# Optimization experiments

Measured on AMD Instinct MI355X. Metric: run time of the kernel, lower is better.

## Reference

```python
import jax, jax.numpy as jnp
import numpy as np

K = 8  # avg_kernel (pool kernel == stride, and nearest-upsample factor)


def conv1x1(u, W, b):
    # 1x1 conv == per-pixel linear map over channels
    return jnp.einsum('bchw,oc->bohw', u, W) + b[None, :, None, None]


def setup_inputs() -> dict:
    key = jax.random.key(0)
    ks = jax.random.split(key, 9)
    C = 64
    x = jax.random.normal(ks[0], (8, C, 512, 512), dtype=jnp.float32)
    def w(k):
        return jax.random.normal(k, (C, C), dtype=jnp.float32) * 0.05
    def bias(k):
        return jax.random.normal(k, (C,), dtype=jnp.float32) * 0.05
    return {
        'x': x,
        'Wt': w(ks[1]), 'bt': bias(ks[2]),
        'Wp': w(ks[3]), 'bp': bias(ks[4]),
        'Wg': w(ks[5]), 'bg': bias(ks[6]),
        'Wc': w(ks[7]), 'bc': bias(ks[8]),
    }


def reference(x, Wt, bt, Wp, bp, Wg, bg, Wc, bc):
    B, C, H, W = x.shape
    # AvgPool2d(kernel=K, stride=K): exact reshape-mean since H,W divisible by K
    u = x.reshape(B, C, H // K, K, W // K, K).mean(axis=(3, 5))  # [B,C,h,w]
    b_, c_, h, w_ = u.shape
    N = h * w_
    theta = conv1x1(u, Wt, bt).reshape(B, C, N).transpose(0, 2, 1)  # [B,N,C]
    phi = conv1x1(u, Wp, bp).reshape(B, C, N)                       # [B,C,N] (downsample = flatten)
    g = conv1x1(u, Wg, bg).reshape(B, C, N).transpose(0, 2, 1)      # [B,N,C]
    attn = jax.nn.softmax(jnp.einsum('bnc,bcm->bnm', theta, phi), axis=-1)  # [B,N,N], unscaled
    y = jnp.einsum('bnm,bmc->bnc', attn, g)                         # [B,N,C]
    y = y.transpose(0, 2, 1).reshape(B, C, h, w_)
    y = conv1x1(y, Wc, bc)
    # F.interpolate(size=[H,W]) default nearest; integer factor K -> exact repeat
    y = jnp.repeat(jnp.repeat(y, K, axis=2), K, axis=3)
    return y
```

## Files before the change

kernel.cpp:

```cpp
#include <hip/hip_runtime.h>
#include <hip/hip_bf16.h>


typedef short short8 __attribute__((ext_vector_type(8)));
typedef float floatx4 __attribute__((ext_vector_type(4)));

__device__ inline unsigned short f2bf(float f) {
    union { float f; unsigned int u; } v; v.f = f;
    unsigned int u = v.u;
    u += 0x7fff + ((u >> 16) & 1);
    return (unsigned short)(u >> 16);
}

__device__ inline float rowsum16(float x) {
    x += __int_as_float(__builtin_amdgcn_update_dpp(0, __float_as_int(x), 0x121, 0xf, 0xf, false));
    x += __int_as_float(__builtin_amdgcn_update_dpp(0, __float_as_int(x), 0x122, 0xf, 0xf, false));
    x += __int_as_float(__builtin_amdgcn_update_dpp(0, __float_as_int(x), 0x124, 0xf, 0xf, false));
    x += __int_as_float(__builtin_amdgcn_update_dpp(0, __float_as_int(x), 0x128, 0xf, 0xf, false));
    return x;
}

__global__ __launch_bounds__(256) void k_pool(const float* __restrict__ x,
                                              float* __restrict__ u) {
    int id = blockIdx.x * 256 + threadIdx.x;
    int ow = id & 63;
    int oh = (id >> 6) & 63;
    int bc = id >> 12;
    const float* p = x + ((size_t)bc * 512 + oh * 8) * 512 + ow * 8;
    float s = 0.f;
#pragma unroll
    for (int r = 0; r < 8; ++r) {
        const float4* q = (const float4*)(p + r * 512);
        float4 a = q[0], b = q[1];
        s += a.x + a.y + a.z + a.w + b.x + b.y + b.z + b.w;
    }
    u[id] = s * (1.f / 64.f);
}

__global__ __launch_bounds__(256) void k_qkv(const float* __restrict__ u,
    const float* __restrict__ Wt, const float* __restrict__ bt,
    const float* __restrict__ Wp, const float* __restrict__ bp,
    const float* __restrict__ Wg, const float* __restrict__ bg,
    unsigned short* __restrict__ th, unsigned short* __restrict__ ph,
    unsigned short* __restrict__ gT) {
    __shared__ float U[64 * 66];
    __shared__ float WtT[64 * 64];
    __shared__ float WpT[64 * 64];
    int b = blockIdx.x >> 6;
    int n0 = (blockIdx.x & 63) * 64;
    int t = threadIdx.x;
#pragma unroll
    for (int i = 0; i < 4; ++i) {
        int f4 = t + 256 * i;
        int cin = f4 >> 4, pos = f4 & 15;
        float4 v = *(const float4*)(u + ((size_t)(b * 64 + cin)) * 4096 + n0 + pos * 4);
        U[cin * 66 + pos * 4 + 0] = v.x;
        U[cin * 66 + pos * 4 + 1] = v.y;
        U[cin * 66 + pos * 4 + 2] = v.z;
        U[cin * 66 + pos * 4 + 3] = v.w;
    }
#pragma unroll
    for (int i = 0; i < 16; ++i) {
        int idx = t + 256 * i;
        int co = idx & 63, ci = idx >> 6;
        WtT[ci * 64 + co] = Wt[co * 64 + ci];
        WpT[ci * 64 + co] = Wp[co * 64 + ci];
    }
    __syncthreads();
    int cO = t & 63, wv = t >> 6;
#pragma unroll 4
    for (int i = 0; i < 16; ++i) {
        int nl = wv + 4 * i;
        float at = bt[cO], ap = bp[cO];
#pragma unroll
        for (int cin = 0; cin < 64; ++cin) {
            float uv = U[cin * 66 + nl];
            at += WtT[cin * 64 + cO] * uv;
            ap += WpT[cin * 64 + cO] * uv;
        }
        size_t o = ((size_t)(b * 4096 + n0 + nl)) * 64 + cO;
        th[o] = f2bf(at);
        ph[o] = f2bf(ap);
    }
#pragma unroll 4
    for (int i = 0; i < 16; ++i) {
        int c = wv + 4 * i;
        float ag = bg[c];
#pragma unroll
        for (int cin = 0; cin < 64; ++cin)
            ag += Wg[c * 64 + cin] * U[cin * 66 + (t & 63)];
        gT[((size_t)(b * 64 + c)) * 4096 + n0 + (t & 63)] = f2bf(ag);
    }
}

__global__ __launch_bounds__(256) void k_attn(
    const unsigned short* __restrict__ th,
    const unsigned short* __restrict__ ph,
    const unsigned short* __restrict__ gT,
    float* __restrict__ y) {
    __shared__ unsigned short Th[64 * 72];
    __shared__ unsigned short Ph[2][64 * 72];
    __shared__ unsigned short Gt[2][64 * 72];
    __shared__ unsigned short Pl[4 * 16 * 72];
    int b = blockIdx.x >> 6;
    int n0 = (blockIdx.x & 63) * 64;
    int t = threadIdx.x;
    int wave = t >> 6, lane = t & 63, quad = lane >> 4, l16 = lane & 15;
    int row = t >> 2, cg = t & 3;

    {
        const unsigned short* src = th + ((size_t)(b * 4096 + n0 + row)) * 64;
        *(short8*)(Th + row * 72 + cg * 8)      = *(const short8*)(src + cg * 8);
        *(short8*)(Th + row * 72 + 32 + cg * 8) = *(const short8*)(src + 32 + cg * 8);
        const unsigned short* sp = ph + ((size_t)(b * 4096 + row)) * 64;
        *(short8*)(Ph[0] + row * 72 + cg * 8)      = *(const short8*)(sp + cg * 8);
        *(short8*)(Ph[0] + row * 72 + 32 + cg * 8) = *(const short8*)(sp + 32 + cg * 8);
        const unsigned short* sg = gT + ((size_t)(b * 64 + row)) * 4096;
        *(short8*)(Gt[0] + row * 72 + cg * 8)      = *(const short8*)(sg + cg * 8);
        *(short8*)(Gt[0] + row * 72 + 32 + cg * 8) = *(const short8*)(sg + 32 + cg * 8);
    }
    __syncthreads();
    short8 a0 = *(const short8*)(Th + (wave * 16 + l16) * 72 + quad * 8);
    short8 a1 = *(const short8*)(Th + (wave * 16 + l16) * 72 + 32 + quad * 8);

    floatx4 Yacc[4];
#pragma unroll
    for (int ct = 0; ct < 4; ++ct) Yacc[ct] = (floatx4){0.f, 0.f, 0.f, 0.f};
    float l[4] = {0.f, 0.f, 0.f, 0.f};

    int cur = 0;
    for (int mt = 0; mt < 64; ++mt) {
        int mn = ((mt + 1) & 63) * 64;
        short8 r0, r1, r2, r3;
        {
            const unsigned short* sp = ph + ((size_t)(b * 4096 + mn + row)) * 64;
            r0 = *(const short8*)(sp + cg * 8);
            r1 = *(const short8*)(sp + 32 + cg * 8);
            const unsigned short* sg = gT + ((size_t)(b * 64 + row)) * 4096 + mn;
            r2 = *(const short8*)(sg + cg * 8);
            r3 = *(const short8*)(sg + 32 + cg * 8);
        }
        const unsigned short* PhC = Ph[cur];
        const unsigned short* GtC = Gt[cur];

        float psum[4] = {0.f, 0.f, 0.f, 0.f};
#pragma unroll
        for (int ct = 0; ct < 4; ++ct) {
            short8 b0 = *(const short8*)(PhC + (ct * 16 + l16) * 72 + quad * 8);
            short8 b1 = *(const short8*)(PhC + (ct * 16 + l16) * 72 + 32 + quad * 8);
            floatx4 acc = (floatx4){0.f, 0.f, 0.f, 0.f};
            __builtin_amdgcn_s_setprio(1);
            acc = __builtin_amdgcn_mfma_f32_16x16x32_bf16(a0, b0, acc, 0, 0, 0);
            acc = __builtin_amdgcn_mfma_f32_16x16x32_bf16(a1, b1, acc, 0, 0, 0);
            __builtin_amdgcn_s_setprio(0);
#pragma unroll
            for (int r = 0; r < 4; ++r) {
                float e = __expf(acc[r]);
                psum[r] += e;
                Pl[wave * 16 * 72 + (quad * 4 + r) * 72 + ct * 16 + l16] = f2bf(e);
            }
        }
#pragma unroll
        for (int r = 0; r < 4; ++r) l[r] += rowsum16(psum[r]);
        short8 p0 = *(const short8*)(Pl + wave * 16 * 72 + l16 * 72 + quad * 8);
        short8 p1 = *(const short8*)(Pl + wave * 16 * 72 + l16 * 72 + 32 + quad * 8);
        __builtin_amdgcn_s_setprio(1);
#pragma unroll
        for (int ct = 0; ct < 4; ++ct) {
            short8 g0 = *(const short8*)(GtC + (ct * 16 + l16) * 72 + quad * 8);
            short8 g1 = *(const short8*)(GtC + (ct * 16 + l16) * 72 + 32 + quad * 8);
            Yacc[ct] = __builtin_amdgcn_mfma_f32_16x16x32_bf16(p0, g0, Yacc[ct], 0, 0, 0);
            Yacc[ct] = __builtin_amdgcn_mfma_f32_16x16x32_bf16(p1, g1, Yacc[ct], 0, 0, 0);
        }
        __builtin_amdgcn_s_setprio(0);
        unsigned short* PhN = Ph[cur ^ 1];
        unsigned short* GtN = Gt[cur ^ 1];
        *(short8*)(PhN + row * 72 + cg * 8)      = r0;
        *(short8*)(PhN + row * 72 + 32 + cg * 8) = r1;
        *(short8*)(GtN + row * 72 + cg * 8)      = r2;
        *(short8*)(GtN + row * 72 + 32 + cg * 8) = r3;
        __syncthreads();
        cur ^= 1;
    }
#pragma unroll
    for (int ct = 0; ct < 4; ++ct)
#pragma unroll
        for (int r = 0; r < 4; ++r) {
            int rr = n0 + wave * 16 + quad * 4 + r;
            y[((size_t)(b * 4096 + rr)) * 64 + ct * 16 + l16] = Yacc[ct][r] / l[r];
        }
}

__global__ __launch_bounds__(256) void k_out(const float* __restrict__ y,
    const float* __restrict__ Wc, const float* __restrict__ bc,
    float* __restrict__ out) {
    __shared__ float Y[64 * 66];
    int b = blockIdx.x >> 6;
    int oh = blockIdx.x & 63;
    int t = threadIdx.x;
#pragma unroll
    for (int i = 0; i < 4; ++i) {
        int f4 = t + 256 * i;
        int w = f4 >> 4, cgp = f4 & 15;
        float4 v = *(const float4*)(y + ((size_t)(b * 4096 + oh * 64 + w)) * 64 + cgp * 4);
        Y[(cgp * 4 + 0) * 66 + w] = v.x;
        Y[(cgp * 4 + 1) * 66 + w] = v.y;
        Y[(cgp * 4 + 2) * 66 + w] = v.z;
        Y[(cgp * 4 + 3) * 66 + w] = v.w;
    }
    __syncthreads();
    int w = t & 63, wv = t >> 6;
#pragma unroll 2
    for (int i = 0; i < 16; ++i) {
        int c = wv + 4 * i;
        float acc = bc[c];
#pragma unroll
        for (int cin = 0; cin < 64; ++cin)
            acc += Wc[c * 64 + cin] * Y[cin * 66 + w];
        float4 v4 = {acc, acc, acc, acc};
        float* base = out + (((size_t)(b * 64 + c)) * 512 + oh * 8) * 512 + w * 8;
#pragma unroll
        for (int r = 0; r < 8; ++r) {
            *(float4*)(base + (size_t)r * 512) = v4;
            *(float4*)(base + (size_t)r * 512 + 4) = v4;
        }
    }
}

extern "C" void kernel_launch(void* const* d_in, const int* in_sizes, int n_in,
                              void* d_out, int out_size, void* d_ws, size_t ws_size,
                              hipStream_t stream) {
    const float* x  = (const float*)d_in[0];
    const float* Wt = (const float*)d_in[1];
    const float* bt = (const float*)d_in[2];
    const float* Wp = (const float*)d_in[3];
    const float* bp = (const float*)d_in[4];
    const float* Wg = (const float*)d_in[5];
    const float* bg = (const float*)d_in[6];
    const float* Wc = (const float*)d_in[7];
    const float* bc = (const float*)d_in[8];
    float* out = (float*)d_out;
    char* ws = (char*)d_ws;
    float* u            = (float*)(ws);
    unsigned short* th  = (unsigned short*)(ws + (8  << 20));
    unsigned short* ph  = (unsigned short*)(ws + (12 << 20));
    unsigned short* gT  = (unsigned short*)(ws + (16 << 20));
    float* y            = (float*)(ws + (20 << 20));

    hipLaunchKernelGGL(k_pool, dim3(8192), dim3(256), 0, stream, x, u);
    hipLaunchKernelGGL(k_qkv,  dim3(512),  dim3(256), 0, stream,
                       u, Wt, bt, Wp, bp, Wg, bg, th, ph, gT);
    hipLaunchKernelGGL(k_attn, dim3(512),  dim3(256), 0, stream, th, ph, gT, y);
    hipLaunchKernelGGL(k_out,  dim3(512),  dim3(256), 0, stream, y, Wc, bc, out);
}
```

Measured before the change: 1.244 ms.

## Restructure QKV projection to hold pixel inputs in registers and use wave-uniform weights

The 1x1-conv projection kernel now gives each lane one pixel's 64 input channels in registers, transposed through LDS. Each wave computes a wave-uniform block of output channels, so weight reads become scalar/broadcast loads and the shared-memory weight transposes go away. Theta and phi results are packed as bf16 pairs in LDS and written out as 16-byte vector stores instead of scattered 2-byte stores. This adds register pressure (64 floats per lane) and more syncs, and it only touches the small projection stage, not the attention kernel.

```diff
diff --git a/kernel.cpp b/kernel.cpp
--- a/kernel.cpp
+++ b/kernel.cpp
@@ -43,53 +43,69 @@
     const float* __restrict__ Wg, const float* __restrict__ bg,
     unsigned short* __restrict__ th, unsigned short* __restrict__ ph,
     unsigned short* __restrict__ gT) {
-    __shared__ float U[64 * 66];
-    __shared__ float WtT[64 * 64];
-    __shared__ float WpT[64 * 64];
+    __shared__ float U[64 * 68];
     int b = blockIdx.x >> 6;
     int n0 = (blockIdx.x & 63) * 64;
     int t = threadIdx.x;
+    int lane = t & 63, wv = t >> 6;
 #pragma unroll
     for (int i = 0; i < 4; ++i) {
         int f4 = t + 256 * i;
         int cin = f4 >> 4, pos = f4 & 15;
         float4 v = *(const float4*)(u + ((size_t)(b * 64 + cin)) * 4096 + n0 + pos * 4);
-        U[cin * 66 + pos * 4 + 0] = v.x;
-        U[cin * 66 + pos * 4 + 1] = v.y;
-        U[cin * 66 + pos * 4 + 2] = v.z;
-        U[cin * 66 + pos * 4 + 3] = v.w;
-    }
-#pragma unroll
+        U[(pos * 4 + 0) * 68 + cin] = v.x;
+        U[(pos * 4 + 1) * 68 + cin] = v.y;
+        U[(pos * 4 + 2) * 68 + cin] = v.z;
+        U[(pos * 4 + 3) * 68 + cin] = v.w;
+    }
+    __syncthreads();
+    float4 ur[16];
+#pragma unroll
+    for (int q = 0; q < 16; ++q) ur[q] = *(const float4*)&U[lane * 68 + q * 4];
+    __syncthreads();
+    unsigned* T = (unsigned*)U;
+    int cb = __builtin_amdgcn_readfirstlane(wv * 16);
+    size_t gbase = (size_t)(b * 64) * 4096 + n0 + lane;
+    float atp = 0.f, app = 0.f;
+#pragma unroll 2
     for (int i = 0; i < 16; ++i) {
-        int idx = t + 256 * i;
-        int co = idx & 63, ci = idx >> 6;
-        WtT[ci * 64 + co] = Wt[co * 64 + ci];
-        WpT[ci * 64 + co] = Wp[co * 64 + ci];
-    }
-    __syncthreads();
-    int cO = t & 63, wv = t >> 6;
-#pragma unroll 4
-    for (int i = 0; i < 16; ++i) {
-        int nl = wv + 4 * i;
-        float at = bt[cO], ap = bp[cO];
-#pragma unroll
-        for (int cin = 0; cin < 64; ++cin) {
-            float uv = U[cin * 66 + nl];
-            at += WtT[cin * 64 + cO] * uv;
-            ap += WpT[cin * 64 + cO] * uv;
-        }
-        size_t o = ((size_t)(b * 4096 + n0 + nl)) * 64 + cO;
-        th[o] = f2bf(at);
-        ph[o] = f2bf(ap);
-    }
-#pragma unroll 4
-    for (int i = 0; i < 16; ++i) {
-        int c = wv + 4 * i;
-        float ag = bg[c];
-#pragma unroll
-        for (int cin = 0; cin < 64; ++cin)
-            ag += Wg[c * 64 + cin] * U[cin * 66 + (t & 63)];
-        gT[((size_t)(b * 64 + c)) * 4096 + n0 + (t & 63)] = f2bf(ag);
+        int cout = cb + i;
+        const float* wt = Wt + cout * 64;
+        const float* wp = Wp + cout * 64;
+        const float* wg = Wg + cout * 64;
+        float t0 = bt[cout], t1 = 0.f;
+        float q0 = bp[cout], q1 = 0.f;
+        float g0 = bg[cout], g1 = 0.f;
+#pragma unroll
+        for (int q = 0; q < 16; ++q) {
+            float4 x = ur[q];
+            if (q & 1) {
+                t1 = fmaf(wt[4*q+3], x.w, fmaf(wt[4*q+2], x.z, fmaf(wt[4*q+1], x.y, fmaf(wt[4*q], x.x, t1))));
+                q1 = fmaf(wp[4*q+3], x.w, fmaf(wp[4*q+2], x.z, fmaf(wp[4*q+1], x.y, fmaf(wp[4*q], x.x, q1))));
+                g1 = fmaf(wg[4*q+3], x.w, fmaf(wg[4*q+2], x.z, fmaf(wg[4*q+1], x.y, fmaf(wg[4*q], x.x, g1))));
+            } else {
+                t0 = fmaf(wt[4*q+3], x.w, fmaf(wt[4*q+2], x.z, fmaf(wt[4*q+1], x.y, fmaf(wt[4*q], x.x, t0))));
+                q0 = fmaf(wp[4*q+3], x.w, fmaf(wp[4*q+2], x.z, fmaf(wp[4*q+1], x.y, fmaf(wp[4*q], x.x, q0))));
+                g0 = fmaf(wg[4*q+3], x.w, fmaf(wg[4*q+2], x.z, fmaf(wg[4*q+1], x.y, fmaf(wg[4*q], x.x, g0))));
+            }
+        }
+        float at = t0 + t1, ap = q0 + q1, ag = g0 + g1;
+        gT[gbase + (size_t)cout * 4096] = f2bf(ag);
+        if (i & 1) {
+            T[lane * 68 + wv * 8 + (i >> 1)]      = (unsigned)f2bf(atp) | ((unsigned)f2bf(at) << 16);
+            T[lane * 68 + 32 + wv * 8 + (i >> 1)] = (unsigned)f2bf(app) | ((unsigned)f2bf(ap) << 16);
+        } else { atp = at; app = ap; }
+    }
+    __syncthreads();
+#pragma unroll
+    for (int j = 0; j < 2; ++j) {
+        int qi = t + 256 * j;
+        int r = qi >> 3, c4 = qi & 7;
+        uint4 vt = *(const uint4*)&T[r * 68 + c4 * 4];
+        uint4 vp = *(const uint4*)&T[r * 68 + 32 + c4 * 4];
+        size_t o = ((size_t)(b * 4096 + n0 + r)) * 64 + c4 * 8;
+        *(uint4*)(th + o) = vt;
+        *(uint4*)(ph + o) = vp;
     }
 }
 
```

New measurement: 1.234 ms (median of 2 runs). About the same (-0.8%).
